# Kernel tuning notes

Hardware: AMD Instinct MI355X
Metric: run time of the kernel (lower is better)

Reference implementation:

```python
import jax, jax.numpy as jnp
import numpy as np

N_NODES = 50000
N_EDGES = 300000
D_NODE = 128
D_EDGE = 128
D_HID = 256
D_OUT = 128


def setup_inputs() -> dict:
    key = jax.random.key(0)
    k1, k2, k3, k4, k5, k6, k7 = jax.random.split(key, 7)
    node_attr = jax.random.normal(k1, (N_NODES, D_NODE), dtype=jnp.float32)
    edge_contact_attr = jax.random.normal(k2, (N_EDGES, D_EDGE), dtype=jnp.float32)
    edge_contact_index = jax.random.randint(k3, (2, N_EDGES), 0, N_NODES, dtype=jnp.int32)
    d_in = 2 * D_NODE + D_EDGE  # 384: [sender, receiver, edge] concat
    W1 = jax.random.normal(k4, (d_in, D_HID), dtype=jnp.float32) / jnp.sqrt(jnp.float32(d_in))
    b1 = jnp.zeros((D_HID,), dtype=jnp.float32)
    W2 = jax.random.normal(k5, (D_HID, D_OUT), dtype=jnp.float32) / jnp.sqrt(jnp.float32(D_HID))
    b2 = jnp.zeros((D_OUT,), dtype=jnp.float32)
    ln_gamma = jnp.ones((D_OUT,), dtype=jnp.float32)
    ln_beta = jnp.zeros((D_OUT,), dtype=jnp.float32)
    return {
        "node_attr": node_attr,
        "edge_contact_attr": edge_contact_attr,
        "edge_contact_index": edge_contact_index,
        "W1": W1, "b1": b1, "W2": W2, "b2": b2,
        "ln_gamma": ln_gamma, "ln_beta": ln_beta,
    }


def _layer_norm(x, gamma, beta, eps=1e-5):
    mu = jnp.mean(x, axis=-1, keepdims=True)
    var = jnp.var(x, axis=-1, keepdims=True)
    return (x - mu) * jax.lax.rsqrt(var + eps) * gamma + beta


def reference(node_attr, edge_contact_attr, edge_contact_index,
              W1, b1, W2, b2, ln_gamma, ln_beta):
    senders_idx = edge_contact_index[0]
    receivers_idx = edge_contact_index[1]
    senders_attr = node_attr[senders_idx]      # [E, D_NODE] gather
    receivers_attr = node_attr[receivers_idx]  # [E, D_NODE] gather
    edge_messages = jnp.concatenate(
        [senders_attr, receivers_attr, edge_contact_attr], axis=1)  # [E, 384]
    h = jax.nn.relu(edge_messages @ W1 + b1)   # [E, D_HID]
    h = h @ W2 + b2                            # [E, D_OUT]
    new_edge_contact_attr = _layer_norm(h, ln_gamma, ln_beta)
    return new_edge_contact_attr
```

## Files before the change

### kernel.cpp

```cpp
#include <hip/hip_runtime.h>

#define E_TOT   300000
#define DN      128
#define DOUT    128

typedef float  f32x4  __attribute__((ext_vector_type(4)));
typedef __bf16 bf16x8 __attribute__((ext_vector_type(8)));

__device__ __forceinline__ unsigned short f2bf(float f) {
    union { float f; unsigned int u; } v; v.f = f;
    return (unsigned short)((v.u + 0x7FFFu + ((v.u >> 16) & 1u)) >> 16);
}

__global__ void prep_weights(const float* __restrict__ W1,
                             const float* __restrict__ W2,
                             unsigned short* __restrict__ W1p,
                             unsigned short* __restrict__ W2p) {
    int t = blockIdx.x * 256 + threadIdx.x;
    if (t < 384 * 256) {
        int k = t >> 8, n = t & 255;
        W1p[(((k >> 6) << 8) + n) * 64 + (k & 63)] = f2bf(W1[t]);
    } else {
        int t2 = t - 384 * 256;
        int k = t2 >> 7, n = t2 & 127;
        W2p[(((k >> 6) << 7) + n) * 64 + (k & 63)] = f2bf(W2[t2]);
    }
}

__global__ __launch_bounds__(256, 3) void edge_mlp(
    const float* __restrict__ node_attr,
    const float* __restrict__ edge_attr,
    const int*   __restrict__ eidx,
    const unsigned short* __restrict__ W1p,
    const unsigned short* __restrict__ W2p,
    const float* __restrict__ b1,
    const float* __restrict__ b2,
    const float* __restrict__ ln_g,
    const float* __restrict__ ln_b,
    float* __restrict__ out)
{
    __shared__ __align__(16) unsigned short smem[26112];
    __shared__ int sIdx[64], rIdx[64];

    unsigned short* Xc   = smem;
    unsigned short* W1c  = smem + 4608;
    unsigned short* hbuf = smem;
    unsigned short* W2c  = smem + 16896;

    const int tid  = threadIdx.x;
    const int wid  = tid >> 6;
    const int lane = tid & 63;
    const int quad = lane >> 4;
    const int l16  = lane & 15;
    const int eb   = blockIdx.x * 64;

    if (tid < 128) {
        int r = tid & 63;
        int e = eb + r; if (e >= E_TOT) e = E_TOT - 1;
        if (tid < 64) sIdx[r] = eidx[e];
        else          rIdx[r] = eidx[E_TOT + e];
    }

    f32x4 acc[4][4];
    #pragma unroll
    for (int i = 0; i < 4; ++i)
        #pragma unroll
        for (int j = 0; j < 4; ++j)
            acc[i][j] = (f32x4){0.f, 0.f, 0.f, 0.f};

    __syncthreads();

    #pragma unroll 1
    for (int c = 0; c < 6; ++c) {
        if (c) __syncthreads();
        const int coloff = (c & 1) << 6;
        #pragma unroll
        for (int i = 0; i < 4; ++i) {
            int id  = (i << 8) + tid;
            int row = id >> 4;
            int q4  = id & 15;
            const float* src;
            if (c < 2)      src = node_attr + (size_t)sIdx[row] * DN;
            else if (c < 4) src = node_attr + (size_t)rIdx[row] * DN;
            else {
                int e = eb + row; if (e >= E_TOT) e = E_TOT - 1;
                src = edge_attr + (size_t)e * DN;
            }
            float4 v = *(const float4*)(src + coloff + (q4 << 2));
            ushort4 p;
            p.x = f2bf(v.x); p.y = f2bf(v.y); p.z = f2bf(v.z); p.w = f2bf(v.w);
            *(ushort4*)(Xc + row * 72 + (q4 << 2)) = p;
        }
        const unsigned short* wsrc = W1p + c * (256 * 64);
        #pragma unroll
        for (int i = 0; i < 8; ++i) {
            int id = (i << 8) + tid;
            *(uint4*)(W1c + (id >> 3) * 72 + ((id & 7) << 3)) =
                *(const uint4*)(wsrc + (id << 3));
        }
        __syncthreads();
        #pragma unroll
        for (int ks = 0; ks < 2; ++ks) {
            bf16x8 a[4];
            #pragma unroll
            for (int mt = 0; mt < 4; ++mt)
                a[mt] = *(const bf16x8*)(Xc + ((mt << 4) + l16) * 72 + (ks << 5) + (quad << 3));
            #pragma unroll
            for (int nt = 0; nt < 4; ++nt) {
                bf16x8 b = *(const bf16x8*)(W1c + ((wid << 6) + (nt << 4) + l16) * 72 + (ks << 5) + (quad << 3));
                #pragma unroll
                for (int mt = 0; mt < 4; ++mt)
                    acc[mt][nt] = __builtin_amdgcn_mfma_f32_16x16x32_bf16(a[mt], b, acc[mt][nt], 0, 0, 0);
            }
        }
    }

    float b1v[4];
    #pragma unroll
    for (int nt = 0; nt < 4; ++nt) b1v[nt] = b1[(wid << 6) + (nt << 4) + l16];
    __syncthreads();
    #pragma unroll
    for (int mt = 0; mt < 4; ++mt)
        #pragma unroll
        for (int nt = 0; nt < 4; ++nt)
            #pragma unroll
            for (int r = 0; r < 4; ++r) {
                int row = (mt << 4) + (quad << 2) + r;
                int col = (wid << 6) + (nt << 4) + l16;
                float v = acc[mt][nt][r] + b1v[nt];
                hbuf[row * 264 + col] = f2bf(v > 0.f ? v : 0.f);
            }
    __syncthreads();

    f32x4 acc2[8];
    #pragma unroll
    for (int nt = 0; nt < 8; ++nt) acc2[nt] = (f32x4){0.f, 0.f, 0.f, 0.f};

    #pragma unroll 1
    for (int c2 = 0; c2 < 4; ++c2) {
        if (c2) __syncthreads();
        const unsigned short* wsrc = W2p + c2 * (128 * 64);
        #pragma unroll
        for (int i = 0; i < 4; ++i) {
            int id = (i << 8) + tid;
            *(uint4*)(W2c + (id >> 3) * 72 + ((id & 7) << 3)) =
                *(const uint4*)(wsrc + (id << 3));
        }
        __syncthreads();
        #pragma unroll
        for (int ks = 0; ks < 2; ++ks) {
            bf16x8 a = *(const bf16x8*)(hbuf + ((wid << 4) + l16) * 264 + (c2 << 6) + (ks << 5) + (quad << 3));
            #pragma unroll
            for (int nt = 0; nt < 8; ++nt) {
                bf16x8 b = *(const bf16x8*)(W2c + ((nt << 4) + l16) * 72 + (ks << 5) + (quad << 3));
                acc2[nt] = __builtin_amdgcn_mfma_f32_16x16x32_bf16(a, b, acc2[nt], 0, 0, 0);
            }
        }
    }

    float b2v[8], gv[8], bev[8];
    #pragma unroll
    for (int nt = 0; nt < 8; ++nt) {
        int n = (nt << 4) + l16;
        b2v[nt] = b2[n]; gv[nt] = ln_g[n]; bev[nt] = ln_b[n];
    }
    #pragma unroll
    for (int r = 0; r < 4; ++r) {
        int e = eb + (wid << 4) + (quad << 2) + r;
        float x[8];
        float s = 0.f, s2 = 0.f;
        #pragma unroll
        for (int nt = 0; nt < 8; ++nt) {
            x[nt] = acc2[nt][r] + b2v[nt];
            s += x[nt]; s2 += x[nt] * x[nt];
        }
        #pragma unroll
        for (int m = 1; m < 16; m <<= 1) {
            s  += __shfl_xor(s, m, 64);
            s2 += __shfl_xor(s2, m, 64);
        }
        const float mu  = s * (1.f / 128.f);
        const float var = s2 * (1.f / 128.f) - mu * mu;
        const float rs  = rsqrtf(var + 1e-5f);
        if (e < E_TOT) {
            float* orow = out + (size_t)e * DOUT;
            #pragma unroll
            for (int nt = 0; nt < 8; ++nt)
                orow[(nt << 4) + l16] = (x[nt] - mu) * rs * gv[nt] + bev[nt];
        }
    }
}

extern "C" void kernel_launch(void* const* d_in, const int* in_sizes, int n_in,
                              void* d_out, int out_size, void* d_ws, size_t ws_size,
                              hipStream_t stream) {
    const float* node_attr = (const float*)d_in[0];
    const float* edge_attr = (const float*)d_in[1];
    const int*   eidx      = (const int*)d_in[2];
    const float* W1        = (const float*)d_in[3];
    const float* b1        = (const float*)d_in[4];
    const float* W2        = (const float*)d_in[5];
    const float* b2        = (const float*)d_in[6];
    const float* ln_g      = (const float*)d_in[7];
    const float* ln_b      = (const float*)d_in[8];

    unsigned short* W1p = (unsigned short*)d_ws;
    unsigned short* W2p = W1p + 384 * 256;

    prep_weights<<<512, 256, 0, stream>>>(W1, W2, W1p, W2p);

    const int nblocks = (E_TOT + 63) / 64;
    edge_mlp<<<nblocks, 256, 0, stream>>>(node_attr, edge_attr, eidx,
                                          W1p, W2p, b1, b2, ln_g, ln_b,
                                          (float*)d_out);
}
```

Measured before the change: 417.1 us.

## Pre-swizzle weights into MFMA fragment order and double-buffer gathered inputs

Weights are now repacked by the prep kernel into per-lane MFMA fragment order, so the main kernel reads B operands straight from global/L2 instead of staging W1/W2 tiles through LDS. This drops the weight staging loops and several barriers, and shrinks shared memory enough to raise launch bounds to 4 blocks per CU. The node/edge gather for the next K chunk is issued before the MFMAs of the current chunk into a second LDS buffer, overlapping gather latency with compute. In exchange, every block now reads weight fragments from global memory on each use, which relies on L2/L1 hit rates.

```diff
diff --git a/kernel.cpp b/kernel.cpp
--- a/kernel.cpp
+++ b/kernel.cpp
@@ -1,8 +1,7 @@
 #include <hip/hip_runtime.h>
-
-#define E_TOT   300000
-#define DN      128
-#define DOUT    128
+#include <hip/hip_bf16.h>
+
+#define E_TOT 300000
 
 typedef float  f32x4  __attribute__((ext_vector_type(4)));
 typedef __bf16 bf16x8 __attribute__((ext_vector_type(8)));
@@ -12,40 +11,59 @@
     return (unsigned short)((v.u + 0x7FFFu + ((v.u >> 16) & 1u)) >> 16);
 }
 
+__device__ __forceinline__ unsigned int packbf2(float x, float y) {
+    __hip_bfloat162 h = __float22bfloat162_rn(make_float2(x, y));
+    union { __hip_bfloat162 h; unsigned int u; } cv; cv.h = h;
+    return cv.u;
+}
+
 __global__ void prep_weights(const float* __restrict__ W1,
                              const float* __restrict__ W2,
-                             unsigned short* __restrict__ W1p,
-                             unsigned short* __restrict__ W2p) {
+                             unsigned short* __restrict__ W1q,
+                             unsigned short* __restrict__ W2q) {
     int t = blockIdx.x * 256 + threadIdx.x;
-    if (t < 384 * 256) {
-        int k = t >> 8, n = t & 255;
-        W1p[(((k >> 6) << 8) + n) * 64 + (k & 63)] = f2bf(W1[t]);
+    if (t < 98304) {
+        int j    = t & 7;
+        int lane = (t >> 3) & 63;
+        int ks   = (t >> 9) & 1;
+        int nt   = (t >> 10) & 3;
+        int w    = (t >> 12) & 3;
+        int c    = t >> 14;
+        int quad = lane >> 4, l16 = lane & 15;
+        int k = c * 64 + ks * 32 + quad * 8 + j;
+        int n = w * 64 + nt * 16 + l16;
+        W1q[t] = f2bf(W1[k * 256 + n]);
     } else {
-        int t2 = t - 384 * 256;
-        int k = t2 >> 7, n = t2 & 127;
-        W2p[(((k >> 6) << 7) + n) * 64 + (k & 63)] = f2bf(W2[t2]);
-    }
-}
-
-__global__ __launch_bounds__(256, 3) void edge_mlp(
+        int t2   = t - 98304;
+        int j    = t2 & 7;
+        int lane = (t2 >> 3) & 63;
+        int nt   = (t2 >> 9) & 7;
+        int ks   = (t2 >> 12) & 1;
+        int c2   = t2 >> 13;
+        int quad = lane >> 4, l16 = lane & 15;
+        int k = c2 * 64 + ks * 32 + quad * 8 + j;
+        int n = nt * 16 + l16;
+        W2q[t2] = f2bf(W2[k * 128 + n]);
+    }
+}
+
+__global__ __launch_bounds__(256, 4) void edge_mlp(
     const float* __restrict__ node_attr,
     const float* __restrict__ edge_attr,
     const int*   __restrict__ eidx,
-    const unsigned short* __restrict__ W1p,
-    const unsigned short* __restrict__ W2p,
+    const unsigned short* __restrict__ W1q,
+    const unsigned short* __restrict__ W2q,
     const float* __restrict__ b1,
     const float* __restrict__ b2,
     const float* __restrict__ ln_g,
     const float* __restrict__ ln_b,
     float* __restrict__ out)
 {
-    __shared__ __align__(16) unsigned short smem[26112];
+    __shared__ __align__(16) unsigned short smem[16896];
     __shared__ int sIdx[64], rIdx[64];
-
-    unsigned short* Xc   = smem;
-    unsigned short* W1c  = smem + 4608;
-    unsigned short* hbuf = smem;
-    unsigned short* W2c  = smem + 16896;
+    unsigned short* const Xc0  = smem;
+    unsigned short* const Xc1  = smem + 4608;
+    unsigned short* const hbuf = smem;
 
     const int tid  = threadIdx.x;
     const int wid  = tid >> 6;
@@ -53,6 +71,8 @@
     const int quad = lane >> 4;
     const int l16  = lane & 15;
     const int eb   = blockIdx.x * 64;
+    const int grow = tid >> 4;
+    const int q4   = tid & 15;
 
     if (tid < 128) {
         int r = tid & 63;
@@ -61,6 +81,10 @@
         else          rIdx[r] = eidx[E_TOT + e];
     }
 
+    float b1v[4];
+    #pragma unroll
+    for (int nt = 0; nt < 4; ++nt) b1v[nt] = b1[(wid << 6) + (nt << 4) + l16];
+
     f32x4 acc[4][4];
     #pragma unroll
     for (int i = 0; i < 4; ++i)
@@ -70,55 +94,64 @@
 
     __syncthreads();
 
+    auto gather = [&](int cc, float4* v) {
+        const int coloff = (cc & 1) << 6;
+        #pragma unroll
+        for (int i = 0; i < 4; ++i) {
+            int row = (i << 4) + grow;
+            const float* src;
+            if (cc < 2)      src = node_attr + (size_t)sIdx[row] * 128;
+            else if (cc < 4) src = node_attr + (size_t)rIdx[row] * 128;
+            else {
+                int e = eb + row; if (e >= E_TOT) e = E_TOT - 1;
+                src = edge_attr + (size_t)e * 128;
+            }
+            v[i] = *(const float4*)(src + coloff + (q4 << 2));
+        }
+    };
+    auto store_x = [&](unsigned short* xb, const float4* v) {
+        #pragma unroll
+        for (int i = 0; i < 4; ++i) {
+            int row = (i << 4) + grow;
+            union { unsigned int u[2]; ushort4 s; } p;
+            p.u[0] = packbf2(v[i].x, v[i].y);
+            p.u[1] = packbf2(v[i].z, v[i].w);
+            *(ushort4*)(xb + row * 72 + (q4 << 2)) = p.s;
+        }
+    };
+
+    {
+        float4 v[4];
+        gather(0, v);
+        store_x(Xc0, v);
+    }
+    __syncthreads();
+
     #pragma unroll 1
     for (int c = 0; c < 6; ++c) {
-        if (c) __syncthreads();
-        const int coloff = (c & 1) << 6;
-        #pragma unroll
-        for (int i = 0; i < 4; ++i) {
-            int id  = (i << 8) + tid;
-            int row = id >> 4;
-            int q4  = id & 15;
-            const float* src;
-            if (c < 2)      src = node_attr + (size_t)sIdx[row] * DN;
-            else if (c < 4) src = node_attr + (size_t)rIdx[row] * DN;
-            else {
-                int e = eb + row; if (e >= E_TOT) e = E_TOT - 1;
-                src = edge_attr + (size_t)e * DN;
-            }
-            float4 v = *(const float4*)(src + coloff + (q4 << 2));
-            ushort4 p;
-            p.x = f2bf(v.x); p.y = f2bf(v.y); p.z = f2bf(v.z); p.w = f2bf(v.w);
-            *(ushort4*)(Xc + row * 72 + (q4 << 2)) = p;
-        }
-        const unsigned short* wsrc = W1p + c * (256 * 64);
-        #pragma unroll
-        for (int i = 0; i < 8; ++i) {
-            int id = (i << 8) + tid;
-            *(uint4*)(W1c + (id >> 3) * 72 + ((id & 7) << 3)) =
-                *(const uint4*)(wsrc + (id << 3));
-        }
-        __syncthreads();
+        const unsigned short* xb = (c & 1) ? Xc1 : Xc0;
+        unsigned short*       xn = (c & 1) ? Xc0 : Xc1;
+        float4 v[4];
+        if (c < 5) gather(c + 1, v);
         #pragma unroll
         for (int ks = 0; ks < 2; ++ks) {
             bf16x8 a[4];
             #pragma unroll
             for (int mt = 0; mt < 4; ++mt)
-                a[mt] = *(const bf16x8*)(Xc + ((mt << 4) + l16) * 72 + (ks << 5) + (quad << 3));
+                a[mt] = *(const bf16x8*)(xb + ((mt << 4) + l16) * 72 + (ks << 5) + (quad << 3));
             #pragma unroll
             for (int nt = 0; nt < 4; ++nt) {
-                bf16x8 b = *(const bf16x8*)(W1c + ((wid << 6) + (nt << 4) + l16) * 72 + (ks << 5) + (quad << 3));
+                bf16x8 b = *(const bf16x8*)(W1q
+                    + (((((c << 2) + wid) << 2) + nt) * 2 + ks) * 512 + (lane << 3));
                 #pragma unroll
                 for (int mt = 0; mt < 4; ++mt)
                     acc[mt][nt] = __builtin_amdgcn_mfma_f32_16x16x32_bf16(a[mt], b, acc[mt][nt], 0, 0, 0);
             }
         }
-    }
-
-    float b1v[4];
-    #pragma unroll
-    for (int nt = 0; nt < 4; ++nt) b1v[nt] = b1[(wid << 6) + (nt << 4) + l16];
-    __syncthreads();
+        if (c < 5) store_x(xn, v);
+        __syncthreads();
+    }
+
     #pragma unroll
     for (int mt = 0; mt < 4; ++mt)
         #pragma unroll
@@ -127,8 +160,8 @@
             for (int r = 0; r < 4; ++r) {
                 int row = (mt << 4) + (quad << 2) + r;
                 int col = (wid << 6) + (nt << 4) + l16;
-                float v = acc[mt][nt][r] + b1v[nt];
-                hbuf[row * 264 + col] = f2bf(v > 0.f ? v : 0.f);
+                float hv = acc[mt][nt][r] + b1v[nt];
+                hbuf[row * 264 + col] = f2bf(hv > 0.f ? hv : 0.f);
             }
     __syncthreads();
 
@@ -138,21 +171,13 @@
 
     #pragma unroll 1
     for (int c2 = 0; c2 < 4; ++c2) {
-        if (c2) __syncthreads();
-        const unsigned short* wsrc = W2p + c2 * (128 * 64);
-        #pragma unroll
-        for (int i = 0; i < 4; ++i) {
-            int id = (i << 8) + tid;
-            *(uint4*)(W2c + (id >> 3) * 72 + ((id & 7) << 3)) =
-                *(const uint4*)(wsrc + (id << 3));
-        }
-        __syncthreads();
         #pragma unroll
         for (int ks = 0; ks < 2; ++ks) {
             bf16x8 a = *(const bf16x8*)(hbuf + ((wid << 4) + l16) * 264 + (c2 << 6) + (ks << 5) + (quad << 3));
             #pragma unroll
             for (int nt = 0; nt < 8; ++nt) {
-                bf16x8 b = *(const bf16x8*)(W2c + ((nt << 4) + l16) * 72 + (ks << 5) + (quad << 3));
+                bf16x8 b = *(const bf16x8*)(W2q
+                    + ((((c2 << 1) + ks) << 3) + nt) * 512 + (lane << 3));
                 acc2[nt] = __builtin_amdgcn_mfma_f32_16x16x32_bf16(a, b, acc2[nt], 0, 0, 0);
             }
         }
@@ -183,7 +208,7 @@
         const float var = s2 * (1.f / 128.f) - mu * mu;
         const float rs  = rsqrtf(var + 1e-5f);
         if (e < E_TOT) {
-            float* orow = out + (size_t)e * DOUT;
+            float* orow = out + (size_t)e * 128;
             #pragma unroll
             for (int nt = 0; nt < 8; ++nt)
                 orow[(nt << 4) + l16] = (x[nt] - mu) * rs * gv[nt] + bev[nt];
@@ -204,13 +229,13 @@
     const float* ln_g      = (const float*)d_in[7];
     const float* ln_b      = (const float*)d_in[8];
 
-    unsigned short* W1p = (unsigned short*)d_ws;
-    unsigned short* W2p = W1p + 384 * 256;
-
-    prep_weights<<<512, 256, 0, stream>>>(W1, W2, W1p, W2p);
+    unsigned short* W1q = (unsigned short*)d_ws;
+    unsigned short* W2q = W1q + 98304;
+
+    prep_weights<<<512, 256, 0, stream>>>(W1, W2, W1q, W2q);
 
     const int nblocks = (E_TOT + 63) / 64;
     edge_mlp<<<nblocks, 256, 0, stream>>>(node_attr, edge_attr, eidx,
-                                          W1p, W2p, b1, b2, ln_g, ln_b,
+                                          W1q, W2q, b1, b2, ln_g, ln_b,
                                           (float*)d_out);
 }
```

Result: slower. 458.9 us (+10.0%).
